# Kernel tuning notes

Measured on AMD Instinct MI355X. Metric: run time of the kernel, lower is better.

The kernel has to match this reference:

```python
import jax, jax.numpy as jnp
import numpy as np

GROUP = 8
BETA = 1.0
LOGVAR_MIN, LOGVAR_MAX = -30.0, 20.0
LOG2PI = float(np.log(2.0 * np.pi))


def setup_inputs() -> dict:
    key = jax.random.key(0)
    k1, k2 = jax.random.split(key)
    # z: [b, c, h, w] with c = 2*latent_c (mu/logvar halves)
    z = jax.random.normal(k1, (4, 64, 64, 64), dtype=jnp.float32)
    # stand-in for the scrambled-Sobol N(0,1) quasi-random codebook [n_samples, group]
    prior_samples = jax.random.normal(k2, (2048, GROUP), dtype=jnp.float32)
    return {"z": z, "prior_samples": prior_samples}


def reference(z, prior_samples):
    z = z.astype(jnp.float32)
    b, c, h, w = z.shape
    l = h * w
    z = z.reshape(b, c, l).transpose(0, 2, 1)          # b (h w) c
    c2 = c // 2
    mu, logvar = z[..., :c2], z[..., c2:]
    logvar = jnp.clip(logvar, LOGVAR_MIN, LOGVAR_MAX)
    std = jnp.exp(0.5 * logvar)
    ng = c2 // GROUP
    # [b, l, group, ng] -> [b, l, ng, group] -> [R, group],  R = b*l*ng
    mu_r = mu.reshape(b, l, GROUP, ng).transpose(0, 1, 3, 2).reshape(-1, GROUP)
    std_r = std.reshape(b, l, GROUP, ng).transpose(0, 1, 3, 2).reshape(-1, GROUP)

    s = prior_samples                                   # [N, G]
    s2 = s * s
    inv_var = 1.0 / (std_r * std_r)                     # [R, G]

    # sum_g Normal(0,1).log_prob(s) per codeword  -> [N]
    nlp_sum = jnp.sum(-0.5 * s2 - 0.5 * LOG2PI, axis=1)

    # score[r,n] = sum_g Normal(mu_r, std_r).log_prob(s[n]) - beta * nlp_sum[n]
    # expanded so the broadcast [R, N, G] tensor is never materialized:
    score = jnp.einsum('rg,ng->rn', -0.5 * inv_var, s2) \
          + jnp.einsum('rg,ng->rn', mu_r * inv_var, s)
    rowconst = (-0.5 * jnp.sum(mu_r * mu_r * inv_var, axis=1)
                - jnp.sum(jnp.log(std_r), axis=1)
                - 0.5 * GROUP * LOG2PI)                 # [R]
    score = score + rowconst[:, None] - BETA * nlp_sum[None, :]

    indices = jnp.argmax(score, axis=1)                 # [R]
    zhat = prior_samples[indices]                       # [R, G]

    zhat = zhat.reshape(b, l, ng, GROUP).transpose(0, 1, 3, 2).reshape(b, l, c2)
    indices = indices.reshape(b, l, ng)
    # back to bchw
    zhat = zhat.transpose(0, 2, 1).reshape(b, c2, h, w)
    indices = indices.transpose(0, 2, 1).reshape(b, ng, h, w)
    return zhat, indices
```

## Files before the change

kernel.cpp:

```cpp
#include <hip/hip_runtime.h>
#include <math.h>

#define L 4096
#define C2 32
#define CTOT 64
#define BB 4
#define NG 4
#define NSAMP 2048
#define TPB 256
#define ROWSPB 64
#define AOFF 196608
#define WS_B 196608
#define WS_A (196608 + 6291456)

typedef _Float16 half8 __attribute__((ext_vector_type(8)));
typedef float f32x16 __attribute__((ext_vector_type(16)));

__device__ __forceinline__ void split3(float x, _Float16& h, _Float16& m, _Float16& l) {
    h = (_Float16)x; float r1 = x - (float)h;
    m = (_Float16)r1; float r2 = r1 - (float)m;
    l = (_Float16)r2;
}

__global__ __launch_bounds__(256) void prep_kernel(
    const float* __restrict__ z, const float* __restrict__ prior,
    char* __restrict__ ws)
{
    const int blk = blockIdx.x, tid = threadIdx.x;
    if (blk < 8) {
        int n = blk * 256 + tid;
        const float4* p4 = (const float4*)prior;
        float4 u = p4[2 * n], v = p4[2 * n + 1];
        float s[8] = {u.x, u.y, u.z, u.w, v.x, v.y, v.z, v.w};
        half8 qh, qm, ql, vh, vm, vl;
        #pragma unroll
        for (int g = 0; g < 8; ++g) {
            _Float16 hh, mm, ll;
            split3(s[g] * s[g], hh, mm, ll);
            qh[g] = hh; qm[g] = mm; ql[g] = ll;
            split3(s[g], hh, mm, ll);
            vh[g] = hh; vm[g] = mm; vl[g] = ll;
        }
        char* tb = ws + (size_t)(n >> 5) * 3072 + (size_t)(n & 31) * 16;
        *(half8*)(tb + 0)    = qh;
        *(half8*)(tb + 512)  = vh;
        *(half8*)(tb + 1024) = qm;
        *(half8*)(tb + 1536) = vm;
        *(half8*)(tb + 2048) = ql;
        *(half8*)(tb + 2560) = vl;
    } else {
        int r = (blk - 8) * 256 + tid;
        int rtg = r >> 5, col = r & 31;
        int b = r >> 14, pos = (r >> 2) & (L - 1), ns = r & 3;
        const float* zb = z + (size_t)b * CTOT * L + pos;
        half8 cah, cam, cal, cbh, cbm, cbl;
        #pragma unroll
        for (int g = 0; g < 8; ++g) {
            float mu = zb[(size_t)(g * NG + ns) * L];
            float lv = zb[(size_t)(C2 + g * NG + ns) * L];
            lv = fminf(fmaxf(lv, -30.f), 20.f);
            float iv = expf(-lv);
            _Float16 hh, mm, ll;
            split3(0.5f - 0.5f * iv, hh, mm, ll);
            cah[g] = hh; cam[g] = mm; cal[g] = ll;
            split3(mu * iv, hh, mm, ll);
            cbh[g] = hh; cbm[g] = mm; cbl[g] = ll;
        }
        char* b0 = ws + AOFF + (size_t)(((rtg * 2 + 0) * 32 + col)) * 48;
        *(half8*)(b0 + 0) = cah; *(half8*)(b0 + 16) = cam; *(half8*)(b0 + 32) = cal;
        char* b1 = ws + AOFF + (size_t)(((rtg * 2 + 1) * 32 + col)) * 48;
        *(half8*)(b1 + 0) = cbh; *(half8*)(b1 + 16) = cbm; *(half8*)(b1 + 32) = cbl;
    }
}

__device__ __forceinline__ void argmax16(const f32x16& acc, int tt,
                                         float* best, int* bt) {
    #pragma unroll
    for (int j = 0; j < 16; ++j) {
        bool gt = acc[j] > best[j];
        best[j] = gt ? acc[j] : best[j];
        bt[j]   = gt ? tt : bt[j];
    }
}

__global__ __launch_bounds__(TPB, 4) void gqreg_main(
    const float* __restrict__ z, const float* __restrict__ prior,
    float* __restrict__ out, const char* __restrict__ wsb, int bws, int aws)
{
    __shared__ float mbB[2][2][2][16];
    __shared__ int   mbI[2][2][2][16];

    const int tid = threadIdx.x;
    const int lane = tid & 63;
    const int w = tid >> 6;
    const int rt = w >> 1;
    const int sh = w & 1;
    const int col = lane & 31;
    const int kh = lane >> 5;
    const float4* p4 = (const float4*)prior;
    const int rowbase = blockIdx.x * ROWSPB + rt * 32;

    half8 ah, am, al;
    if (aws) {
        int rtg = blockIdx.x * 2 + rt;
        const char* ab = wsb + AOFF + (size_t)((rtg * 2 + kh) * 32 + col) * 48;
        ah = *(const half8*)(ab + 0);
        am = *(const half8*)(ab + 16);
        al = *(const half8*)(ab + 32);
    } else {
        int r = rowbase + col;
        int b = r >> 14, pos = (r >> 2) & (L - 1), ns = r & 3;
        const float* zb = z + (size_t)b * CTOT * L + pos;
        #pragma unroll
        for (int g = 0; g < 8; ++g) {
            float mu = zb[(size_t)(g * NG + ns) * L];
            float lv = zb[(size_t)(C2 + g * NG + ns) * L];
            lv = fminf(fmaxf(lv, -30.f), 20.f);
            float iv = expf(-lv);
            float x = kh ? (mu * iv) : (0.5f - 0.5f * iv);
            _Float16 xh, xm, xl;
            split3(x, xh, xm, xl);
            ah[g] = xh; am[g] = xm; al[g] = xl;
        }
    }

    float best[16];
    int bt[16];
    #pragma unroll
    for (int j = 0; j < 16; ++j) { best[j] = -INFINITY; bt[j] = 0; }
    const f32x16 z16 = {};

#define CHAIN(dst, Bh_, Bm_, Bl_)                                              \
    do {                                                                       \
        __builtin_amdgcn_s_setprio(1);                                         \
        dst = __builtin_amdgcn_mfma_f32_32x32x16_f16(ah, Bh_, z16, 0, 0, 0);   \
        dst = __builtin_amdgcn_mfma_f32_32x32x16_f16(ah, Bm_, dst, 0, 0, 0);   \
        dst = __builtin_amdgcn_mfma_f32_32x32x16_f16(am, Bh_, dst, 0, 0, 0);   \
        dst = __builtin_amdgcn_mfma_f32_32x32x16_f16(am, Bm_, dst, 0, 0, 0);   \
        dst = __builtin_amdgcn_mfma_f32_32x32x16_f16(ah, Bl_, dst, 0, 0, 0);   \
        dst = __builtin_amdgcn_mfma_f32_32x32x16_f16(al, Bh_, dst, 0, 0, 0);   \
        __builtin_amdgcn_s_setprio(0);                                         \
    } while (0)

    if (bws) {
        const char* base = wsb + (size_t)(sh * 32) * 3072 + (size_t)(kh * 512 + col * 16);
        const int tbase = sh * 32;
        half8 Xh, Xm, Xl, Yh, Ym, Yl;
        f32x16 aA, aB;
        Xh = *(const half8*)(base + 0);
        Xm = *(const half8*)(base + 1024);
        Xl = *(const half8*)(base + 2048);
        #pragma unroll
        for (int i = 0; i < 16; ++i) {
            {
                const char* q = base + (size_t)(2 * i + 1) * 3072;
                Yh = *(const half8*)(q + 0);
                Ym = *(const half8*)(q + 1024);
                Yl = *(const half8*)(q + 2048);
            }
            if (i > 0) argmax16(aB, tbase + 2 * i - 1, best, bt);
            CHAIN(aA, Xh, Xm, Xl);
            if (i + 1 < 16) {
                const char* q = base + (size_t)(2 * i + 2) * 3072;
                Xh = *(const half8*)(q + 0);
                Xm = *(const half8*)(q + 1024);
                Xl = *(const half8*)(q + 2048);
            }
            CHAIN(aB, Yh, Ym, Yl);
            argmax16(aA, tbase + 2 * i, best, bt);
        }
        argmax16(aB, tbase + 31, best, bt);
    } else {
        #pragma unroll 2
        for (int t = 0; t < 32; ++t) {
            const int tt = sh * 32 + t;
            int n = tt * 32 + col;
            float4 u = p4[2 * n], v = p4[2 * n + 1];
            float sv[8] = {u.x, u.y, u.z, u.w, v.x, v.y, v.z, v.w};
            half8 Bh, Bm, Bl;
            #pragma unroll
            for (int g = 0; g < 8; ++g) {
                float x = kh ? sv[g] : sv[g] * sv[g];
                _Float16 hh, mm, ll;
                split3(x, hh, mm, ll);
                Bh[g] = hh; Bm[g] = mm; Bl[g] = ll;
            }
            f32x16 acc;
            CHAIN(acc, Bh, Bm, Bl);
            argmax16(acc, tt, best, bt);
        }
    }
#undef CHAIN

    int bn[16];
    #pragma unroll
    for (int j = 0; j < 16; ++j) bn[j] = bt[j] * 32 + col;
    #pragma unroll
    for (int j = 0; j < 16; ++j) {
        #pragma unroll
        for (int m = 1; m < 32; m <<= 1) {
            float os = __shfl_xor(best[j], m, 64);
            int oi = __shfl_xor(bn[j], m, 64);
            if (os > best[j] || (os == best[j] && oi < bn[j])) {
                best[j] = os; bn[j] = oi;
            }
        }
    }

    if (col == 0) {
        #pragma unroll
        for (int j = 0; j < 16; ++j) {
            mbB[rt][sh][kh][j] = best[j];
            mbI[rt][sh][kh][j] = bn[j];
        }
    }
    __syncthreads();

    if (w == 0) {
        int rt_o = lane >> 5;
        int rr = lane & 31;
        int kh_o = (rr >> 2) & 1;
        int j_o = (rr & 3) | ((rr >> 3) << 2);
        float b0 = mbB[rt_o][0][kh_o][j_o];
        int i0 = mbI[rt_o][0][kh_o][j_o];
        float b1 = mbB[rt_o][1][kh_o][j_o];
        int i1 = mbI[rt_o][1][kh_o][j_o];
        int n = (b1 > b0) ? i1 : i0;
        int r = blockIdx.x * ROWSPB + rt_o * 32 + rr;
        int b = r >> 14, pos = (r >> 2) & (L - 1), ns = r & 3;
        out[(size_t)BB * C2 * L + ((size_t)b * NG + ns) * L + pos] = (float)n;
        float4 uu = p4[2 * n], vv = p4[2 * n + 1];
        float sv[8] = {uu.x, uu.y, uu.z, uu.w, vv.x, vv.y, vv.z, vv.w};
        #pragma unroll
        for (int g = 0; g < 8; ++g) {
            out[((size_t)b * C2 + g * NG + ns) * L + pos] = sv[g];
        }
    }
}

extern "C" void kernel_launch(void* const* d_in, const int* in_sizes, int n_in,
                              void* d_out, int out_size, void* d_ws, size_t ws_size,
                              hipStream_t stream) {
    const float* z = (const float*)d_in[0];
    const float* prior = (const float*)d_in[1];
    float* out = (float*)d_out;
    char* ws = (char*)d_ws;
    int bws = (ws_size >= (size_t)WS_B) ? 1 : 0;
    int aws = (ws_size >= (size_t)WS_A) ? 1 : 0;

    if (bws) {
        int nprep = 8 + (aws ? 256 : 0);
        hipLaunchKernelGGL(prep_kernel, dim3(nprep), dim3(256), 0, stream,
                           z, prior, ws);
    }
    hipLaunchKernelGGL(gqreg_main, dim3((BB * L * NG) / ROWSPB), dim3(TPB), 0, stream,
                       z, prior, out, (const char*)ws, bws, aws);
}
```

Baseline: 46.02 us.

## Drop A-operand prepass and deepen B-operand prefetch to three buffers

Removes the workspace prepass that split the z-derived A operands into fp16 triples, so the main kernel now always computes them inline from z. This avoids writing and re-reading about 6 MB of workspace. The codeword B-operand loop moves from double to triple buffering, giving loads more lead time ahead of the MFMA chains. The occupancy hint in launch_bounds is also dropped. The cost is more registers and extra inline exp and split work in every block.

```diff
diff --git a/kernel.cpp b/kernel.cpp
--- a/kernel.cpp
+++ b/kernel.cpp
@@ -9,9 +9,7 @@
 #define NSAMP 2048
 #define TPB 256
 #define ROWSPB 64
-#define AOFF 196608
 #define WS_B 196608
-#define WS_A (196608 + 6291456)
 
 typedef _Float16 half8 __attribute__((ext_vector_type(8)));
 typedef float f32x16 __attribute__((ext_vector_type(16)));
@@ -22,55 +20,29 @@
     l = (_Float16)r2;
 }
 
-__global__ __launch_bounds__(256) void prep_kernel(
-    const float* __restrict__ z, const float* __restrict__ prior,
-    char* __restrict__ ws)
+__global__ __launch_bounds__(256) void presplit_kernel(
+    const float* __restrict__ prior, char* __restrict__ ws)
 {
-    const int blk = blockIdx.x, tid = threadIdx.x;
-    if (blk < 8) {
-        int n = blk * 256 + tid;
-        const float4* p4 = (const float4*)prior;
-        float4 u = p4[2 * n], v = p4[2 * n + 1];
-        float s[8] = {u.x, u.y, u.z, u.w, v.x, v.y, v.z, v.w};
-        half8 qh, qm, ql, vh, vm, vl;
-        #pragma unroll
-        for (int g = 0; g < 8; ++g) {
-            _Float16 hh, mm, ll;
-            split3(s[g] * s[g], hh, mm, ll);
-            qh[g] = hh; qm[g] = mm; ql[g] = ll;
-            split3(s[g], hh, mm, ll);
-            vh[g] = hh; vm[g] = mm; vl[g] = ll;
-        }
-        char* tb = ws + (size_t)(n >> 5) * 3072 + (size_t)(n & 31) * 16;
-        *(half8*)(tb + 0)    = qh;
-        *(half8*)(tb + 512)  = vh;
-        *(half8*)(tb + 1024) = qm;
-        *(half8*)(tb + 1536) = vm;
-        *(half8*)(tb + 2048) = ql;
-        *(half8*)(tb + 2560) = vl;
-    } else {
-        int r = (blk - 8) * 256 + tid;
-        int rtg = r >> 5, col = r & 31;
-        int b = r >> 14, pos = (r >> 2) & (L - 1), ns = r & 3;
-        const float* zb = z + (size_t)b * CTOT * L + pos;
-        half8 cah, cam, cal, cbh, cbm, cbl;
-        #pragma unroll
-        for (int g = 0; g < 8; ++g) {
-            float mu = zb[(size_t)(g * NG + ns) * L];
-            float lv = zb[(size_t)(C2 + g * NG + ns) * L];
-            lv = fminf(fmaxf(lv, -30.f), 20.f);
-            float iv = expf(-lv);
-            _Float16 hh, mm, ll;
-            split3(0.5f - 0.5f * iv, hh, mm, ll);
-            cah[g] = hh; cam[g] = mm; cal[g] = ll;
-            split3(mu * iv, hh, mm, ll);
-            cbh[g] = hh; cbm[g] = mm; cbl[g] = ll;
-        }
-        char* b0 = ws + AOFF + (size_t)(((rtg * 2 + 0) * 32 + col)) * 48;
-        *(half8*)(b0 + 0) = cah; *(half8*)(b0 + 16) = cam; *(half8*)(b0 + 32) = cal;
-        char* b1 = ws + AOFF + (size_t)(((rtg * 2 + 1) * 32 + col)) * 48;
-        *(half8*)(b1 + 0) = cbh; *(half8*)(b1 + 16) = cbm; *(half8*)(b1 + 32) = cbl;
-    }
+    int n = blockIdx.x * 256 + threadIdx.x;
+    const float4* p4 = (const float4*)prior;
+    float4 u = p4[2 * n], v = p4[2 * n + 1];
+    float s[8] = {u.x, u.y, u.z, u.w, v.x, v.y, v.z, v.w};
+    half8 qh, qm, ql, vh, vm, vl;
+    #pragma unroll
+    for (int g = 0; g < 8; ++g) {
+        _Float16 hh, mm, ll;
+        split3(s[g] * s[g], hh, mm, ll);
+        qh[g] = hh; qm[g] = mm; ql[g] = ll;
+        split3(s[g], hh, mm, ll);
+        vh[g] = hh; vm[g] = mm; vl[g] = ll;
+    }
+    char* tb = ws + (size_t)(n >> 5) * 3072 + (size_t)(n & 31) * 16;
+    *(half8*)(tb + 0)    = qh;
+    *(half8*)(tb + 512)  = vh;
+    *(half8*)(tb + 1024) = qm;
+    *(half8*)(tb + 1536) = vm;
+    *(half8*)(tb + 2048) = ql;
+    *(half8*)(tb + 2560) = vl;
 }
 
 __device__ __forceinline__ void argmax16(const f32x16& acc, int tt,
@@ -83,9 +55,9 @@
     }
 }
 
-__global__ __launch_bounds__(TPB, 4) void gqreg_main(
+__global__ __launch_bounds__(TPB) void gqreg_main(
     const float* __restrict__ z, const float* __restrict__ prior,
-    float* __restrict__ out, const char* __restrict__ wsb, int bws, int aws)
+    float* __restrict__ out, const char* __restrict__ wsb, int bws)
 {
     __shared__ float mbB[2][2][2][16];
     __shared__ int   mbI[2][2][2][16];
@@ -101,13 +73,7 @@
     const int rowbase = blockIdx.x * ROWSPB + rt * 32;
 
     half8 ah, am, al;
-    if (aws) {
-        int rtg = blockIdx.x * 2 + rt;
-        const char* ab = wsb + AOFF + (size_t)((rtg * 2 + kh) * 32 + col) * 48;
-        ah = *(const half8*)(ab + 0);
-        am = *(const half8*)(ab + 16);
-        al = *(const half8*)(ab + 32);
-    } else {
+    {
         int r = rowbase + col;
         int b = r >> 14, pos = (r >> 2) & (L - 1), ns = r & 3;
         const float* zb = z + (size_t)b * CTOT * L + pos;
@@ -142,33 +108,42 @@
         __builtin_amdgcn_s_setprio(0);                                         \
     } while (0)
 
+#define LOADB(Bh_, Bm_, Bl_, t_)                                               \
+    do {                                                                       \
+        const char* q_ = base + (size_t)(t_) * 3072;                           \
+        Bh_ = *(const half8*)(q_ + 0);                                         \
+        Bm_ = *(const half8*)(q_ + 1024);                                      \
+        Bl_ = *(const half8*)(q_ + 2048);                                      \
+    } while (0)
+
     if (bws) {
         const char* base = wsb + (size_t)(sh * 32) * 3072 + (size_t)(kh * 512 + col * 16);
         const int tbase = sh * 32;
-        half8 Xh, Xm, Xl, Yh, Ym, Yl;
+        half8 Ph, Pm, Pl, Qh, Qm, Ql, Rh, Rm, Rl;
         f32x16 aA, aB;
-        Xh = *(const half8*)(base + 0);
-        Xm = *(const half8*)(base + 1024);
-        Xl = *(const half8*)(base + 2048);
-        #pragma unroll
-        for (int i = 0; i < 16; ++i) {
-            {
-                const char* q = base + (size_t)(2 * i + 1) * 3072;
-                Yh = *(const half8*)(q + 0);
-                Ym = *(const half8*)(q + 1024);
-                Yl = *(const half8*)(q + 2048);
-            }
-            if (i > 0) argmax16(aB, tbase + 2 * i - 1, best, bt);
-            CHAIN(aA, Xh, Xm, Xl);
-            if (i + 1 < 16) {
-                const char* q = base + (size_t)(2 * i + 2) * 3072;
-                Xh = *(const half8*)(q + 0);
-                Xm = *(const half8*)(q + 1024);
-                Xl = *(const half8*)(q + 2048);
-            }
-            CHAIN(aB, Yh, Ym, Yl);
-            argmax16(aA, tbase + 2 * i, best, bt);
-        }
+        LOADB(Ph, Pm, Pl, 0);
+        LOADB(Qh, Qm, Ql, 1);
+        LOADB(Rh, Rm, Rl, 2);
+        for (int i = 0; i < 5; ++i) {
+            const int t0 = 6 * i;
+            CHAIN(aA, Ph, Pm, Pl);  LOADB(Ph, Pm, Pl, t0 + 3);
+            if (i > 0) argmax16(aB, tbase + t0 - 1, best, bt);
+            CHAIN(aB, Qh, Qm, Ql);  LOADB(Qh, Qm, Ql, t0 + 4);
+            argmax16(aA, tbase + t0, best, bt);
+            CHAIN(aA, Rh, Rm, Rl);  LOADB(Rh, Rm, Rl, t0 + 5);
+            argmax16(aB, tbase + t0 + 1, best, bt);
+            CHAIN(aB, Ph, Pm, Pl);  LOADB(Ph, Pm, Pl, t0 + 6);
+            argmax16(aA, tbase + t0 + 2, best, bt);
+            CHAIN(aA, Qh, Qm, Ql);  LOADB(Qh, Qm, Ql, t0 + 7);
+            argmax16(aB, tbase + t0 + 3, best, bt);
+            CHAIN(aB, Rh, Rm, Rl);
+            if (i < 4) LOADB(Rh, Rm, Rl, t0 + 8);
+            argmax16(aA, tbase + t0 + 4, best, bt);
+        }
+        argmax16(aB, tbase + 29, best, bt);
+        CHAIN(aA, Ph, Pm, Pl);
+        CHAIN(aB, Qh, Qm, Ql);
+        argmax16(aA, tbase + 30, best, bt);
         argmax16(aB, tbase + 31, best, bt);
     } else {
         #pragma unroll 2
@@ -191,6 +166,7 @@
         }
     }
 #undef CHAIN
+#undef LOADB
 
     int bn[16];
     #pragma unroll
@@ -246,13 +222,11 @@
     float* out = (float*)d_out;
     char* ws = (char*)d_ws;
     int bws = (ws_size >= (size_t)WS_B) ? 1 : 0;
-    int aws = (ws_size >= (size_t)WS_A) ? 1 : 0;
 
     if (bws) {
-        int nprep = 8 + (aws ? 256 : 0);
-        hipLaunchKernelGGL(prep_kernel, dim3(nprep), dim3(256), 0, stream,
-                           z, prior, ws);
+        hipLaunchKernelGGL(presplit_kernel, dim3(NSAMP / 256), dim3(256), 0, stream,
+                           prior, ws);
     }
     hipLaunchKernelGGL(gqreg_main, dim3((BB * L * NG) / ROWSPB), dim3(TPB), 0, stream,
-                       z, prior, out, (const char*)ws, bws, aws);
-}
+                       z, prior, out, (const char*)ws, bws);
+}
```

After: 77.63 us. 1.69x slower.
